# Kernel tuning notes

Hardware: AMD Instinct MI355X
Metric: run time of the kernel (lower is better)

The kernel has to match this reference:

```python
import jax, jax.numpy as jnp
import numpy as np


def _l2norm(t, eps=1e-12):
    # matches torch F.normalize(p=2, dim=-1): x / max(||x||_2, eps)
    n = jnp.sqrt(jnp.sum(t * t, axis=-1, keepdims=True))
    return t / jnp.maximum(n, eps)


def setup_inputs() -> dict:
    key = jax.random.key(0)
    ks = jax.random.split(key, 8)
    B, N, C, H, W = 16, 4, 256, 64, 64
    d = 64  # dim_head
    x = jax.random.normal(ks[0], (B, C, H, W), jnp.float32)
    fmaps = jax.random.normal(ks[1], (B, N, C, H, W), jnp.float32)
    Wq = jax.random.normal(ks[2], (N * d, C), jnp.float32) * 0.02   # Linear [out,in]
    Wk = jax.random.normal(ks[3], (N, d, C), jnp.float32) * 0.02    # grouped 1x1 conv, per-group [d,C]
    Wv = jax.random.normal(ks[4], (N, d, C), jnp.float32) * 0.02
    rescale = jnp.ones((N, 1, 1), jnp.float32)
    Wffn = jax.random.normal(ks[5], (C, N * d), jnp.float32) * 0.02
    bffn = jnp.zeros((C,), jnp.float32)
    return {"x": x, "fmaps": fmaps, "Wq": Wq, "Wk": Wk, "Wv": Wv,
            "rescale": rescale, "Wffn": Wffn, "bffn": bffn}


def reference(x, fmaps, Wq, Wk, Wv, rescale, Wffn, bffn):
    B, N, C, H, W = fmaps.shape
    d = Wk.shape[1]
    HW = H * W

    # x: [B,C,H,W] -> tokens [B,HW,C]
    x_in = jnp.transpose(x, (0, 2, 3, 1)).reshape(B, HW, C)
    q_in = jnp.einsum('bsc,oc->bso', x_in, Wq)            # [B,HW,N*d]

    # grouped 1x1 convs on fmaps (group = fmap index n)
    fm = fmaps.reshape(B, N, C, HW)                       # [B,N,C,HW]
    k = jnp.einsum('bncs,ndc->bnds', fm, Wk)              # [B,N,d,HW]
    v = jnp.einsum('bncs,ndc->bnds', fm, Wv)              # [B,N,d,HW]

    q = jnp.transpose(q_in.reshape(B, HW, N, d), (0, 2, 3, 1))  # [B,N,d,HW]

    qn = _l2norm(q)   # normalize over spatial (HW) axis
    kn = _l2norm(k)

    attn = jnp.einsum('bnds,bnes->bnde', kn, qn) * rescale      # [B,N,d,d]
    attn = jax.nn.softmax(attn, axis=-1)
    out = jnp.einsum('bnde,bnes->bnds', attn, v)                # [B,N,d,HW]

    out = jnp.transpose(out, (0, 3, 1, 2)).reshape(B, HW, N * d)  # [B,HW,N*d]
    out = out + q_in
    out = jnp.einsum('bsi,ci->bsc', out, Wffn) + bffn + q_in      # ffn + residual
    return jnp.transpose(out.reshape(B, H, W, C), (0, 3, 1, 2))   # [B,C,H,W]
```

## Files before the change

kernel.cpp:

```cpp
#include <hip/hip_runtime.h>
#include <hip/hip_bf16.h>
#include <cmath>

using bf16 = __hip_bfloat16;
typedef __attribute__((ext_vector_type(4))) float  f32x4;
typedef __attribute__((ext_vector_type(8))) short  bf16x8;
typedef unsigned int u32;
typedef unsigned short u16;

__device__ __forceinline__ void gl_lds16(const bf16* g, bf16* l) {
    __builtin_amdgcn_global_load_lds(
        (const __attribute__((address_space(1))) u32*)g,
        (__attribute__((address_space(3))) u32*)l, 16, 0, 0);
}

__device__ __forceinline__ u32 pk2(float a, float b) {
    bf16 ha = __float2bfloat16(a), hb = __float2bfloat16(b);
    return (u32)*(u16*)&ha | ((u32)*(u16*)&hb << 16);
}
__device__ __forceinline__ float b2f(u16 v) {
    return __uint_as_float((u32)v << 16);
}

__global__ __launch_bounds__(256) void qproj(
    const float* __restrict__ x,
    const bf16* __restrict__ Wq,
    bf16* __restrict__ qch)
{
    __shared__ bf16 sW[128 * 64];
    __shared__ bf16 sX[128 * 72];
    const int t = threadIdx.x;
    const int lane = t & 63, wid = t >> 6;
    const int wm = wid >> 1, wn = wid & 1;
    const int g = lane >> 4, lr = lane & 15;
    const int s0 = blockIdx.x * 128;
    const int o0 = blockIdx.y * 128;
    const float* xb = x + (long)blockIdx.z * 1048576;

    f32x4 acc[4][4];
#pragma unroll
    for (int i = 0; i < 4; ++i)
#pragma unroll
        for (int j = 0; j < 4; ++j) acc[i][j] = (f32x4){0.f, 0.f, 0.f, 0.f};

    const int p  = t & 31;
    const int sl = t >> 5;

    for (int c0 = 0; c0 < 256; c0 += 64) {
        __syncthreads();
#pragma unroll
        for (int i = 0; i < 4; ++i) {
            int lin = i * 256 + t, r = lin >> 3, ch = lin & 7;
            gl_lds16(Wq + (long)(o0 + r) * 256 + c0 + ((ch ^ (r & 7)) << 3), &sW[lin * 8]);
        }
#pragma unroll
        for (int j = 0; j < 4; ++j) {
            int s4 = j * 8 + sl;
            const float* src = xb + (long)(c0 + 2 * p) * 4096 + s0 + s4 * 4;
            float4 a = *(const float4*)src;
            float4 bq = *(const float4*)(src + 4096);
            char* base = (char*)sX + p * 4 + (s4 * 4) * 144;
            *(u32*)(base +   0) = pk2(a.x, bq.x);
            *(u32*)(base + 144) = pk2(a.y, bq.y);
            *(u32*)(base + 288) = pk2(a.z, bq.z);
            *(u32*)(base + 432) = pk2(a.w, bq.w);
        }
        __syncthreads();
#pragma unroll
        for (int kk = 0; kk < 2; ++kk) {
            bf16x8 aw[4], fx[4];
#pragma unroll
            for (int mf = 0; mf < 4; ++mf) {
                int r = wm * 64 + mf * 16 + lr;
                int ch = (kk * 4 + g) ^ (r & 7);
                aw[mf] = *(const bf16x8*)((const char*)sW + r * 128 + ch * 16);
            }
#pragma unroll
            for (int nf = 0; nf < 4; ++nf) {
                int s = wn * 64 + nf * 16 + lr;
                fx[nf] = *(const bf16x8*)((const char*)sX + s * 144 + (kk * 4 + g) * 16);
            }
#pragma unroll
            for (int mf = 0; mf < 4; ++mf)
#pragma unroll
                for (int nf = 0; nf < 4; ++nf)
                    acc[mf][nf] = __builtin_amdgcn_mfma_f32_16x16x32_bf16(
                        aw[mf], fx[nf], acc[mf][nf], 0, 0, 0);
        }
    }
    bf16* qb = qch + (long)blockIdx.z * 1048576;
#pragma unroll
    for (int mf = 0; mf < 4; ++mf)
#pragma unroll
        for (int nf = 0; nf < 4; ++nf)
#pragma unroll
            for (int e = 0; e < 4; ++e) {
                int o = o0 + wm * 64 + mf * 16 + g * 4 + e;
                int s = s0 + wn * 64 + nf * 16 + lr;
                qb[(long)o * 4096 + s] = __float2bfloat16(acc[mf][nf][e]);
            }
}

__global__ __launch_bounds__(256) void kvproj(
    const float* __restrict__ fm,
    const bf16* __restrict__ Wk,
    const bf16* __restrict__ Wv,
    bf16* __restrict__ kb,
    bf16* __restrict__ vT)
{
    __shared__ bf16 sF[128 * 72];
    __shared__ bf16 sK[64 * 64];
    __shared__ bf16 sV[64 * 64];
    const int t = threadIdx.x;
    const int lane = t & 63, wid = t >> 6;
    const int g = lane >> 4, lr = lane & 15;
    const int s0 = blockIdx.x * 128;
    const int bn = blockIdx.y, n = bn & 3;
    const float* fb = fm + (long)bn * 1048576;
    const bf16* WkN = Wk + (long)n * 16384;
    const bf16* WvN = Wv + (long)n * 16384;

    f32x4 acc1[4][2];
    f32x4 acc2[2][4];
#pragma unroll
    for (int i = 0; i < 4; ++i)
#pragma unroll
        for (int j = 0; j < 2; ++j) {
            acc1[i][j] = (f32x4){0.f, 0.f, 0.f, 0.f};
            acc2[j][i] = (f32x4){0.f, 0.f, 0.f, 0.f};
        }

    const int p  = t & 31;
    const int sl = t >> 5;

    for (int c0 = 0; c0 < 256; c0 += 64) {
        __syncthreads();
#pragma unroll
        for (int i = 0; i < 2; ++i) {
            int lin = i * 256 + t, r = lin >> 3, ch = lin & 7;
            int srcoff = r * 256 + c0 + ((ch ^ (r & 7)) << 3);
            gl_lds16(WkN + srcoff, &sK[lin * 8]);
            gl_lds16(WvN + srcoff, &sV[lin * 8]);
        }
#pragma unroll
        for (int j = 0; j < 4; ++j) {
            int s4 = j * 8 + sl;
            const float* src = fb + (long)(c0 + 2 * p) * 4096 + s0 + s4 * 4;
            float4 a = *(const float4*)src;
            float4 bq = *(const float4*)(src + 4096);
            char* base = (char*)sF + p * 4 + (s4 * 4) * 144;
            *(u32*)(base +   0) = pk2(a.x, bq.x);
            *(u32*)(base + 144) = pk2(a.y, bq.y);
            *(u32*)(base + 288) = pk2(a.z, bq.z);
            *(u32*)(base + 432) = pk2(a.w, bq.w);
        }
        __syncthreads();
#pragma unroll
        for (int kk = 0; kk < 2; ++kk) {
            bf16x8 ak[4], ff[2], bv[4];
#pragma unroll
            for (int mf = 0; mf < 4; ++mf) {
                int r = mf * 16 + lr;
                int ch = (kk * 4 + g) ^ (r & 7);
                ak[mf] = *(const bf16x8*)((const char*)sK + r * 128 + ch * 16);
            }
#pragma unroll
            for (int i = 0; i < 2; ++i) {
                int s = wid * 32 + i * 16 + lr;
                ff[i] = *(const bf16x8*)((const char*)sF + s * 144 + (kk * 4 + g) * 16);
            }
#pragma unroll
            for (int nf = 0; nf < 4; ++nf) {
                int r = nf * 16 + lr;
                int ch = (kk * 4 + g) ^ (r & 7);
                bv[nf] = *(const bf16x8*)((const char*)sV + r * 128 + ch * 16);
            }
#pragma unroll
            for (int mf = 0; mf < 4; ++mf)
#pragma unroll
                for (int i = 0; i < 2; ++i)
                    acc1[mf][i] = __builtin_amdgcn_mfma_f32_16x16x32_bf16(
                        ak[mf], ff[i], acc1[mf][i], 0, 0, 0);
#pragma unroll
            for (int i = 0; i < 2; ++i)
#pragma unroll
                for (int nf = 0; nf < 4; ++nf)
                    acc2[i][nf] = __builtin_amdgcn_mfma_f32_16x16x32_bf16(
                        ff[i], bv[nf], acc2[i][nf], 0, 0, 0);
        }
    }
    bf16* kbb = kb + (long)bn * 262144;
#pragma unroll
    for (int mf = 0; mf < 4; ++mf)
#pragma unroll
        for (int i = 0; i < 2; ++i)
#pragma unroll
            for (int e = 0; e < 4; ++e) {
                int dd = mf * 16 + g * 4 + e;
                int s  = s0 + wid * 32 + i * 16 + lr;
                kbb[(long)dd * 4096 + s] = __float2bfloat16(acc1[mf][i][e]);
            }
    bf16* vtb = vT + (long)bn * 262144;
#pragma unroll
    for (int i = 0; i < 2; ++i)
#pragma unroll
        for (int nf = 0; nf < 4; ++nf)
#pragma unroll
            for (int e = 0; e < 4; ++e) {
                int s = s0 + wid * 32 + i * 16 + g * 4 + e;
                int ec = nf * 16 + lr;
                vtb[(long)s * 64 + ec] = __float2bfloat16(acc2[i][nf][e]);
            }
}

__global__ __launch_bounds__(256) void qk_sum(
    const bf16* __restrict__ kb,
    const bf16* __restrict__ qch,
    float* __restrict__ part,
    float* __restrict__ sumq, float* __restrict__ sumk)
{
    __shared__ bf16 sA[64 * 64];
    __shared__ bf16 sB[64 * 64];
    const int t = threadIdx.x;
    const int lane = t & 63, wid = t >> 6;
    const int wm = wid >> 1, wn = wid & 1;
    const int g = lane >> 4, lr = lane & 15;
    const int ch_ = blockIdx.x;
    const int bn = blockIdx.y;
    const bf16* kbase = kb + (long)bn * 262144;
    const bf16* qbase = qch + (long)bn * 262144;

    const int srow = t >> 1;
    const int shalf = t & 1;

    f32x4 acc[2][2];
#pragma unroll
    for (int i = 0; i < 2; ++i)
#pragma unroll
        for (int j = 0; j < 2; ++j) acc[i][j] = (f32x4){0.f, 0.f, 0.f, 0.f};
    float ss = 0.f;

    for (int it = 0; it < 16; ++it) {
        int k0 = ch_ * 1024 + it * 64;
        __syncthreads();
#pragma unroll
        for (int i = 0; i < 2; ++i) {
            int lin = i * 256 + t, r = lin >> 3, c = lin & 7;
            gl_lds16(kbase + (long)r * 4096 + k0 + ((c ^ (r & 7)) << 3), &sA[lin * 8]);
            gl_lds16(qbase + (long)r * 4096 + k0 + ((c ^ (r & 7)) << 3), &sB[lin * 8]);
        }
        __syncthreads();
#pragma unroll
        for (int kk = 0; kk < 2; ++kk) {
            bf16x8 af[2], bf[2];
#pragma unroll
            for (int mf = 0; mf < 2; ++mf) {
                int r = wm * 32 + mf * 16 + lr;
                af[mf] = *(const bf16x8*)((const char*)sA + r * 128 + (((kk * 4 + g) ^ (r & 7)) << 4));
            }
#pragma unroll
            for (int nf = 0; nf < 2; ++nf) {
                int r = wn * 32 + nf * 16 + lr;
                bf[nf] = *(const bf16x8*)((const char*)sB + r * 128 + (((kk * 4 + g) ^ (r & 7)) << 4));
            }
#pragma unroll
            for (int mf = 0; mf < 2; ++mf)
#pragma unroll
                for (int nf = 0; nf < 2; ++nf)
                    acc[mf][nf] = __builtin_amdgcn_mfma_f32_16x16x32_bf16(
                        af[mf], bf[nf], acc[mf][nf], 0, 0, 0);
        }
        {
            const char* base = (srow < 64) ? (const char*)sA + srow * 128
                                           : (const char*)sB + (srow - 64) * 128;
            int r7 = srow & 7;
#pragma unroll
            for (int j = 0; j < 4; ++j) {
                bf16x8 v = *(const bf16x8*)(base + (((shalf * 4 + j) ^ r7) << 4));
#pragma unroll
                for (int e = 0; e < 8; ++e) {
                    float f = b2f((u16)v[e]);
                    ss += f * f;
                }
            }
        }
    }
    ss += __shfl_xor(ss, 1);
    if (shalf == 0) {
        if (srow < 64) atomicAdd(&sumk[bn * 64 + srow], ss);
        else           atomicAdd(&sumq[bn * 64 + srow - 64], ss);
    }
    float* pp = part + ((long)bn * 4 + ch_) * 4096;
#pragma unroll
    for (int mf = 0; mf < 2; ++mf)
#pragma unroll
        for (int nf = 0; nf < 2; ++nf)
#pragma unroll
            for (int e = 0; e < 4; ++e) {
                int m = wm * 32 + mf * 16 + g * 4 + e;
                int nn = wn * 32 + nf * 16 + lr;
                pp[m * 64 + nn] = acc[mf][nf][e];
            }
}

__global__ __launch_bounds__(256) void attn_finalize_kernel(
    const float* __restrict__ part,
    const float* __restrict__ sumq, const float* __restrict__ sumk,
    const float* __restrict__ rescale,
    bf16* __restrict__ attn_out)
{
    const int bn = blockIdx.x;
    const int n = bn & 3;
    const int t = threadIdx.x;
    const float rs = rescale[n];

    __shared__ float att[64][65];
    __shared__ float rmax[64], rsum[64];
    __shared__ float iq[64], ik[64];

    if (t < 64)        ik[t]      = 1.f / fmaxf(sqrtf(sumk[bn * 64 + t]), 1e-12f);
    else if (t < 128)  iq[t - 64] = 1.f / fmaxf(sqrtf(sumq[bn * 64 + t - 64]), 1e-12f);
    __syncthreads();

    const float* pb = part + (size_t)bn * 4 * 4096;
#pragma unroll
    for (int p = 0; p < 16; ++p) {
        int lin = p * 256 + t;
        int dd = lin >> 6, e = lin & 63;
        float v = pb[lin] + pb[4096 + lin] + pb[8192 + lin] + pb[12288 + lin];
        v *= ik[dd] * iq[e] * rs;
        att[dd][e] = v;
    }
    __syncthreads();
    if (t < 64) {
        float m = -1e30f;
        for (int e = 0; e < 64; ++e) m = fmaxf(m, att[t][e]);
        float sm = 0.f;
        for (int e = 0; e < 64; ++e) sm += expf(att[t][e] - m);
        rmax[t] = m;
        rsum[t] = 1.0f / sm;
    }
    __syncthreads();
    bf16* ob = attn_out + (size_t)bn * 4096;
#pragma unroll
    for (int p = 0; p < 16; ++p) {
        int lin = p * 256 + t;
        int dd = lin >> 6, e = lin & 63;
        ob[lin] = __float2bfloat16(expf(att[dd][e] - rmax[dd]) * rsum[dd]);
    }
}

__global__ __launch_bounds__(256) void pvffn(
    const bf16* __restrict__ vT,
    const bf16* __restrict__ attnb,
    const bf16* __restrict__ qch,
    const bf16* __restrict__ Wf,
    const float* __restrict__ bffn,
    float* __restrict__ out)
{
    __shared__ bf16 bufX[256 * 64];
    __shared__ bf16 Zs[128 * 64];
    const int t = threadIdx.x;
    const int lane = t & 63, wid = t >> 6;
    const int g = lane >> 4, lr = lane & 15;
    const int s0 = blockIdx.x * 128;
    const int b = blockIdx.y;

    f32x4 accF[4][8];
#pragma unroll
    for (int i = 0; i < 4; ++i)
#pragma unroll
        for (int j = 0; j < 8; ++j) accF[i][j] = (f32x4){0.f, 0.f, 0.f, 0.f};

    for (int n = 0; n < 4; ++n) {
        const int bn = b * 4 + n;
        __syncthreads();
#pragma unroll
        for (int i = 0; i < 4; ++i) {
            int lin = i * 256 + t, r = lin >> 3, c = lin & 7;
            gl_lds16(vT + (long)bn * 262144 + (long)(s0 + r) * 64 + ((c ^ (r & 7)) << 3),
                     &bufX[lin * 8]);
        }
#pragma unroll
        for (int i = 0; i < 2; ++i) {
            int lin = i * 256 + t, r = lin >> 3, c = lin & 7;
            gl_lds16(attnb + (long)bn * 4096 + r * 64 + ((c ^ (r & 7)) << 3),
                     &bufX[8192 + lin * 8]);
        }
        __syncthreads();
        f32x4 accP[2][4];
#pragma unroll
        for (int i = 0; i < 2; ++i)
#pragma unroll
            for (int j = 0; j < 4; ++j) accP[i][j] = (f32x4){0.f, 0.f, 0.f, 0.f};
#pragma unroll
        for (int kk = 0; kk < 2; ++kk) {
            bf16x8 av[2], at[4];
#pragma unroll
            for (int mf = 0; mf < 2; ++mf) {
                int r = wid * 32 + mf * 16 + lr;
                av[mf] = *(const bf16x8*)((const char*)bufX + r * 128 + (((kk * 4 + g) ^ (r & 7)) << 4));
            }
#pragma unroll
            for (int nf = 0; nf < 4; ++nf) {
                int r = nf * 16 + lr;
                at[nf] = *(const bf16x8*)((const char*)bufX + 16384 + r * 128 + (((kk * 4 + g) ^ (r & 7)) << 4));
            }
#pragma unroll
            for (int mf = 0; mf < 2; ++mf)
#pragma unroll
                for (int nf = 0; nf < 4; ++nf)
                    accP[mf][nf] = __builtin_amdgcn_mfma_f32_16x16x32_bf16(
                        av[mf], at[nf], accP[mf][nf], 0, 0, 0);
        }
#pragma unroll
        for (int mf = 0; mf < 2; ++mf)
#pragma unroll
            for (int nf = 0; nf < 4; ++nf) {
                int slb = wid * 32 + mf * 16 + g * 4;
                int il = nf * 16 + lr;
                ushort4 qv = *(const ushort4*)(qch + ((long)b * 256 + n * 64 + il) * 4096 + s0 + slb);
                u16 qa[4] = {qv.x, qv.y, qv.z, qv.w};
#pragma unroll
                for (int e = 0; e < 4; ++e) {
                    int sl = slb + e;
                    float v = accP[mf][nf][e] + b2f(qa[e]);
                    bf16 hv = __float2bfloat16(v);
                    int byte = sl * 128 + ((((il >> 3) ^ (sl & 7))) << 4) + (il & 7) * 2;
                    *(u16*)((char*)Zs + byte) = *(u16*)&hv;
                }
            }
        __syncthreads();
#pragma unroll
        for (int i = 0; i < 8; ++i) {
            int lin = i * 256 + t, r = lin >> 3, c = lin & 7;
            gl_lds16(Wf + (long)r * 256 + n * 64 + ((c ^ (r & 7)) << 3), &bufX[lin * 8]);
        }
        __syncthreads();
#pragma unroll
        for (int kk = 0; kk < 2; ++kk) {
            bf16x8 aw[4], bz[8];
#pragma unroll
            for (int mf = 0; mf < 4; ++mf) {
                int r = wid * 64 + mf * 16 + lr;
                aw[mf] = *(const bf16x8*)((const char*)bufX + r * 128 + (((kk * 4 + g) ^ (r & 7)) << 4));
            }
#pragma unroll
            for (int nf = 0; nf < 8; ++nf) {
                int sl = nf * 16 + lr;
                bz[nf] = *(const bf16x8*)((const char*)Zs + sl * 128 + (((kk * 4 + g) ^ (sl & 7)) << 4));
            }
#pragma unroll
            for (int mf = 0; mf < 4; ++mf)
#pragma unroll
                for (int nf = 0; nf < 8; ++nf)
                    accF[mf][nf] = __builtin_amdgcn_mfma_f32_16x16x32_bf16(
                        aw[mf], bz[nf], accF[mf][nf], 0, 0, 0);
        }
    }
    float* ob = out + (long)b * 1048576;
    const bf16* qb = qch + (long)b * 1048576;
#pragma unroll
    for (int mf = 0; mf < 4; ++mf)
#pragma unroll
        for (int e = 0; e < 4; ++e) {
            int c = wid * 64 + mf * 16 + g * 4 + e;
            float bv = bffn[c];
#pragma unroll
            for (int nf = 0; nf < 8; ++nf) {
                int s = s0 + nf * 16 + lr;
                long idx = (long)c * 4096 + s;
                ob[idx] = accF[mf][nf][e] + bv + b2f(*(const u16*)(qb + idx));
            }
        }
}

__global__ __launch_bounds__(256) void wconv(
    const float* __restrict__ a, const float* __restrict__ b,
    const float* __restrict__ c, const float* __restrict__ d,
    bf16* __restrict__ o)
{
    int i = blockIdx.x * 256 + threadIdx.x;
    int which = i >> 16, off = i & 65535;
    const float* s = (which == 0) ? a : (which == 1) ? b : (which == 2) ? c : d;
    o[i] = __float2bfloat16(s[off]);
}

extern "C" void kernel_launch(void* const* d_in, const int* in_sizes, int n_in,
                              void* d_out, int out_size, void* d_ws, size_t ws_size,
                              hipStream_t stream) {
    const float* x       = (const float*)d_in[0];
    const float* fmaps   = (const float*)d_in[1];
    const float* Wq      = (const float*)d_in[2];
    const float* Wk      = (const float*)d_in[3];
    const float* Wv      = (const float*)d_in[4];
    const float* rescale = (const float*)d_in[5];
    const float* Wffn    = (const float*)d_in[6];
    const float* bffn    = (const float*)d_in[7];
    float* out = (float*)d_out;

    char* w = (char*)d_ws;
    bf16* kbuf  = (bf16*)(w + 0);
    bf16* vT    = (bf16*)(w + 33554432L);
    bf16* qch   = (bf16*)(w + 67108864L);
    float* part = (float*)(w + 100663296L);
    bf16* attnb = (bf16*)(w + 104857600L);
    float* sumq = (float*)(w + 105381888L);
    float* sumk = (float*)(w + 105398272L);
    bf16* Wq_b  = (bf16*)(w + 105414656L);
    bf16* Wk_b  = Wq_b + 65536;
    bf16* Wv_b  = Wq_b + 131072;
    bf16* Wf_b  = Wq_b + 196608;

    dim3 blk(256);

    hipMemsetAsync(sumq, 0, 32768, stream);
    wconv<<<dim3(1024), blk, 0, stream>>>(Wq, Wk, Wv, Wffn, Wq_b);
    kvproj<<<dim3(32, 64), blk, 0, stream>>>(fmaps, Wk_b, Wv_b, kbuf, vT);
    qproj<<<dim3(32, 2, 16), blk, 0, stream>>>(x, Wq_b, qch);
    qk_sum<<<dim3(4, 64), blk, 0, stream>>>(kbuf, qch, part, sumq, sumk);
    attn_finalize_kernel<<<dim3(64), blk, 0, stream>>>(part, sumq, sumk, rescale, attnb);
    pvffn<<<dim3(32, 16), blk, 0, stream>>>(vT, attnb, qch, Wf_b, bffn, out);
}
```

Before: 200.9 us.

## Double-buffer LDS tiles across projection, QK and PV/FFN kernels

Adds ping-pong shared-memory buffers to qproj, kvproj, qk_sum and pvffn so the next channel or spatial chunk is fetched while MFMAs run on the current one. qk_sum now splits its reduction 8 ways and writes per-chunk partial norms instead of using atomics, which removes the memset; finalize sums the chunks. pvffn loads Wffn fragments straight into registers rather than staging them through LDS. The cost is more LDS per block, which may lower occupancy, plus more register pressure.

```diff
diff --git a/kernel.cpp b/kernel.cpp
--- a/kernel.cpp
+++ b/kernel.cpp
@@ -27,8 +27,8 @@
     const bf16* __restrict__ Wq,
     bf16* __restrict__ qch)
 {
-    __shared__ bf16 sW[128 * 64];
-    __shared__ bf16 sX[128 * 72];
+    __shared__ bf16 sW[2][128 * 64];
+    __shared__ bf16 sX[2][128 * 72];
     const int t = threadIdx.x;
     const int lane = t & 63, wid = t >> 6;
     const int wm = wid >> 1, wn = wid & 1;
@@ -46,39 +46,62 @@
     const int p  = t & 31;
     const int sl = t >> 5;
 
-    for (int c0 = 0; c0 < 256; c0 += 64) {
-        __syncthreads();
+    {
 #pragma unroll
         for (int i = 0; i < 4; ++i) {
             int lin = i * 256 + t, r = lin >> 3, ch = lin & 7;
-            gl_lds16(Wq + (long)(o0 + r) * 256 + c0 + ((ch ^ (r & 7)) << 3), &sW[lin * 8]);
-        }
+            gl_lds16(Wq + (long)(o0 + r) * 256 + ((ch ^ (r & 7)) << 3), &sW[0][lin * 8]);
+        }
+        float4 ra[4], rb[4];
 #pragma unroll
         for (int j = 0; j < 4; ++j) {
-            int s4 = j * 8 + sl;
-            const float* src = xb + (long)(c0 + 2 * p) * 4096 + s0 + s4 * 4;
-            float4 a = *(const float4*)src;
-            float4 bq = *(const float4*)(src + 4096);
-            char* base = (char*)sX + p * 4 + (s4 * 4) * 144;
-            *(u32*)(base +   0) = pk2(a.x, bq.x);
-            *(u32*)(base + 144) = pk2(a.y, bq.y);
-            *(u32*)(base + 288) = pk2(a.z, bq.z);
-            *(u32*)(base + 432) = pk2(a.w, bq.w);
+            const float* src = xb + (long)(2 * p) * 4096 + s0 + (j * 8 + sl) * 4;
+            ra[j] = *(const float4*)src;
+            rb[j] = *(const float4*)(src + 4096);
+        }
+#pragma unroll
+        for (int j = 0; j < 4; ++j) {
+            char* base = (char*)&sX[0][0] + p * 4 + ((j * 8 + sl) * 4) * 144;
+            *(u32*)(base +   0) = pk2(ra[j].x, rb[j].x);
+            *(u32*)(base + 144) = pk2(ra[j].y, rb[j].y);
+            *(u32*)(base + 288) = pk2(ra[j].z, rb[j].z);
+            *(u32*)(base + 432) = pk2(ra[j].w, rb[j].w);
         }
         __syncthreads();
+    }
+
+    int cur = 0;
+    for (int it = 0; it < 4; ++it) {
+        const int c0n = (it + 1) * 64;
+        float4 ra[4], rb[4];
+        if (it < 3) {
+#pragma unroll
+            for (int i = 0; i < 4; ++i) {
+                int lin = i * 256 + t, r = lin >> 3, ch = lin & 7;
+                gl_lds16(Wq + (long)(o0 + r) * 256 + c0n + ((ch ^ (r & 7)) << 3),
+                         &sW[cur ^ 1][lin * 8]);
+            }
+#pragma unroll
+            for (int j = 0; j < 4; ++j) {
+                const float* src = xb + (long)(c0n + 2 * p) * 4096 + s0 + (j * 8 + sl) * 4;
+                ra[j] = *(const float4*)src;
+                rb[j] = *(const float4*)(src + 4096);
+            }
+        }
+        const char* wbase = (const char*)&sW[cur][0];
+        const char* xbase = (const char*)&sX[cur][0];
 #pragma unroll
         for (int kk = 0; kk < 2; ++kk) {
             bf16x8 aw[4], fx[4];
 #pragma unroll
             for (int mf = 0; mf < 4; ++mf) {
                 int r = wm * 64 + mf * 16 + lr;
-                int ch = (kk * 4 + g) ^ (r & 7);
-                aw[mf] = *(const bf16x8*)((const char*)sW + r * 128 + ch * 16);
+                aw[mf] = *(const bf16x8*)(wbase + r * 128 + (((kk * 4 + g) ^ (r & 7)) << 4));
             }
 #pragma unroll
             for (int nf = 0; nf < 4; ++nf) {
                 int s = wn * 64 + nf * 16 + lr;
-                fx[nf] = *(const bf16x8*)((const char*)sX + s * 144 + (kk * 4 + g) * 16);
+                fx[nf] = *(const bf16x8*)(xbase + s * 144 + (kk * 4 + g) * 16);
             }
 #pragma unroll
             for (int mf = 0; mf < 4; ++mf)
@@ -87,7 +110,20 @@
                     acc[mf][nf] = __builtin_amdgcn_mfma_f32_16x16x32_bf16(
                         aw[mf], fx[nf], acc[mf][nf], 0, 0, 0);
         }
-    }
+        if (it < 3) {
+#pragma unroll
+            for (int j = 0; j < 4; ++j) {
+                char* base = (char*)&sX[cur ^ 1][0] + p * 4 + ((j * 8 + sl) * 4) * 144;
+                *(u32*)(base +   0) = pk2(ra[j].x, rb[j].x);
+                *(u32*)(base + 144) = pk2(ra[j].y, rb[j].y);
+                *(u32*)(base + 288) = pk2(ra[j].z, rb[j].z);
+                *(u32*)(base + 432) = pk2(ra[j].w, rb[j].w);
+            }
+            __syncthreads();
+            cur ^= 1;
+        }
+    }
+
     bf16* qb = qch + (long)blockIdx.z * 1048576;
 #pragma unroll
     for (int mf = 0; mf < 4; ++mf)
@@ -108,9 +144,9 @@
     bf16* __restrict__ kb,
     bf16* __restrict__ vT)
 {
-    __shared__ bf16 sF[128 * 72];
-    __shared__ bf16 sK[64 * 64];
-    __shared__ bf16 sV[64 * 64];
+    __shared__ bf16 sF[2][128 * 72];
+    __shared__ bf16 sK[2][64 * 64];
+    __shared__ bf16 sV[2][64 * 64];
     const int t = threadIdx.x;
     const int lane = t & 63, wid = t >> 6;
     const int g = lane >> 4, lr = lane & 15;
@@ -133,47 +169,71 @@
     const int p  = t & 31;
     const int sl = t >> 5;
 
-    for (int c0 = 0; c0 < 256; c0 += 64) {
-        __syncthreads();
+    {
 #pragma unroll
         for (int i = 0; i < 2; ++i) {
             int lin = i * 256 + t, r = lin >> 3, ch = lin & 7;
-            int srcoff = r * 256 + c0 + ((ch ^ (r & 7)) << 3);
-            gl_lds16(WkN + srcoff, &sK[lin * 8]);
-            gl_lds16(WvN + srcoff, &sV[lin * 8]);
-        }
+            int off = r * 256 + ((ch ^ (r & 7)) << 3);
+            gl_lds16(WkN + off, &sK[0][lin * 8]);
+            gl_lds16(WvN + off, &sV[0][lin * 8]);
+        }
+        float4 ra[4], rb[4];
 #pragma unroll
         for (int j = 0; j < 4; ++j) {
-            int s4 = j * 8 + sl;
-            const float* src = fb + (long)(c0 + 2 * p) * 4096 + s0 + s4 * 4;
-            float4 a = *(const float4*)src;
-            float4 bq = *(const float4*)(src + 4096);
-            char* base = (char*)sF + p * 4 + (s4 * 4) * 144;
-            *(u32*)(base +   0) = pk2(a.x, bq.x);
-            *(u32*)(base + 144) = pk2(a.y, bq.y);
-            *(u32*)(base + 288) = pk2(a.z, bq.z);
-            *(u32*)(base + 432) = pk2(a.w, bq.w);
+            const float* src = fb + (long)(2 * p) * 4096 + s0 + (j * 8 + sl) * 4;
+            ra[j] = *(const float4*)src;
+            rb[j] = *(const float4*)(src + 4096);
+        }
+#pragma unroll
+        for (int j = 0; j < 4; ++j) {
+            char* base = (char*)&sF[0][0] + p * 4 + ((j * 8 + sl) * 4) * 144;
+            *(u32*)(base +   0) = pk2(ra[j].x, rb[j].x);
+            *(u32*)(base + 144) = pk2(ra[j].y, rb[j].y);
+            *(u32*)(base + 288) = pk2(ra[j].z, rb[j].z);
+            *(u32*)(base + 432) = pk2(ra[j].w, rb[j].w);
         }
         __syncthreads();
+    }
+
+    int cur = 0;
+    for (int it = 0; it < 4; ++it) {
+        const int c0n = (it + 1) * 64;
+        float4 ra[4], rb[4];
+        if (it < 3) {
+#pragma unroll
+            for (int i = 0; i < 2; ++i) {
+                int lin = i * 256 + t, r = lin >> 3, ch = lin & 7;
+                int off = r * 256 + c0n + ((ch ^ (r & 7)) << 3);
+                gl_lds16(WkN + off, &sK[cur ^ 1][lin * 8]);
+                gl_lds16(WvN + off, &sV[cur ^ 1][lin * 8]);
+            }
+#pragma unroll
+            for (int j = 0; j < 4; ++j) {
+                const float* src = fb + (long)(c0n + 2 * p) * 4096 + s0 + (j * 8 + sl) * 4;
+                ra[j] = *(const float4*)src;
+                rb[j] = *(const float4*)(src + 4096);
+            }
+        }
+        const char* fbase = (const char*)&sF[cur][0];
+        const char* kbase = (const char*)&sK[cur][0];
+        const char* vbase = (const char*)&sV[cur][0];
 #pragma unroll
         for (int kk = 0; kk < 2; ++kk) {
             bf16x8 ak[4], ff[2], bv[4];
 #pragma unroll
             for (int mf = 0; mf < 4; ++mf) {
                 int r = mf * 16 + lr;
-                int ch = (kk * 4 + g) ^ (r & 7);
-                ak[mf] = *(const bf16x8*)((const char*)sK + r * 128 + ch * 16);
+                ak[mf] = *(const bf16x8*)(kbase + r * 128 + (((kk * 4 + g) ^ (r & 7)) << 4));
             }
 #pragma unroll
             for (int i = 0; i < 2; ++i) {
                 int s = wid * 32 + i * 16 + lr;
-                ff[i] = *(const bf16x8*)((const char*)sF + s * 144 + (kk * 4 + g) * 16);
+                ff[i] = *(const bf16x8*)(fbase + s * 144 + (kk * 4 + g) * 16);
             }
 #pragma unroll
             for (int nf = 0; nf < 4; ++nf) {
                 int r = nf * 16 + lr;
-                int ch = (kk * 4 + g) ^ (r & 7);
-                bv[nf] = *(const bf16x8*)((const char*)sV + r * 128 + ch * 16);
+                bv[nf] = *(const bf16x8*)(vbase + r * 128 + (((kk * 4 + g) ^ (r & 7)) << 4));
             }
 #pragma unroll
             for (int mf = 0; mf < 4; ++mf)
@@ -188,7 +248,20 @@
                     acc2[i][nf] = __builtin_amdgcn_mfma_f32_16x16x32_bf16(
                         ff[i], bv[nf], acc2[i][nf], 0, 0, 0);
         }
-    }
+        if (it < 3) {
+#pragma unroll
+            for (int j = 0; j < 4; ++j) {
+                char* base = (char*)&sF[cur ^ 1][0] + p * 4 + ((j * 8 + sl) * 4) * 144;
+                *(u32*)(base +   0) = pk2(ra[j].x, rb[j].x);
+                *(u32*)(base + 144) = pk2(ra[j].y, rb[j].y);
+                *(u32*)(base + 288) = pk2(ra[j].z, rb[j].z);
+                *(u32*)(base + 432) = pk2(ra[j].w, rb[j].w);
+            }
+            __syncthreads();
+            cur ^= 1;
+        }
+    }
+
     bf16* kbb = kb + (long)bn * 262144;
 #pragma unroll
     for (int mf = 0; mf < 4; ++mf)
@@ -219,8 +292,8 @@
     float* __restrict__ part,
     float* __restrict__ sumq, float* __restrict__ sumk)
 {
-    __shared__ bf16 sA[64 * 64];
-    __shared__ bf16 sB[64 * 64];
+    __shared__ bf16 sA[2][64 * 64];
+    __shared__ bf16 sB[2][64 * 64];
     const int t = threadIdx.x;
     const int lane = t & 63, wid = t >> 6;
     const int wm = wid >> 1, wn = wid & 1;
@@ -240,28 +313,42 @@
         for (int j = 0; j < 2; ++j) acc[i][j] = (f32x4){0.f, 0.f, 0.f, 0.f};
     float ss = 0.f;
 
-    for (int it = 0; it < 16; ++it) {
-        int k0 = ch_ * 1024 + it * 64;
-        __syncthreads();
+    {
+        int k0 = ch_ * 512;
 #pragma unroll
         for (int i = 0; i < 2; ++i) {
             int lin = i * 256 + t, r = lin >> 3, c = lin & 7;
-            gl_lds16(kbase + (long)r * 4096 + k0 + ((c ^ (r & 7)) << 3), &sA[lin * 8]);
-            gl_lds16(qbase + (long)r * 4096 + k0 + ((c ^ (r & 7)) << 3), &sB[lin * 8]);
+            gl_lds16(kbase + (long)r * 4096 + k0 + ((c ^ (r & 7)) << 3), &sA[0][lin * 8]);
+            gl_lds16(qbase + (long)r * 4096 + k0 + ((c ^ (r & 7)) << 3), &sB[0][lin * 8]);
         }
         __syncthreads();
+    }
+
+    int cur = 0;
+    for (int it = 0; it < 8; ++it) {
+        if (it < 7) {
+            int k0 = ch_ * 512 + (it + 1) * 64;
+#pragma unroll
+            for (int i = 0; i < 2; ++i) {
+                int lin = i * 256 + t, r = lin >> 3, c = lin & 7;
+                gl_lds16(kbase + (long)r * 4096 + k0 + ((c ^ (r & 7)) << 3), &sA[cur ^ 1][lin * 8]);
+                gl_lds16(qbase + (long)r * 4096 + k0 + ((c ^ (r & 7)) << 3), &sB[cur ^ 1][lin * 8]);
+            }
+        }
+        const char* abase = (const char*)&sA[cur][0];
+        const char* bbase = (const char*)&sB[cur][0];
 #pragma unroll
         for (int kk = 0; kk < 2; ++kk) {
             bf16x8 af[2], bf[2];
 #pragma unroll
             for (int mf = 0; mf < 2; ++mf) {
                 int r = wm * 32 + mf * 16 + lr;
-                af[mf] = *(const bf16x8*)((const char*)sA + r * 128 + (((kk * 4 + g) ^ (r & 7)) << 4));
+                af[mf] = *(const bf16x8*)(abase + r * 128 + (((kk * 4 + g) ^ (r & 7)) << 4));
             }
 #pragma unroll
             for (int nf = 0; nf < 2; ++nf) {
                 int r = wn * 32 + nf * 16 + lr;
-                bf[nf] = *(const bf16x8*)((const char*)sB + r * 128 + (((kk * 4 + g) ^ (r & 7)) << 4));
+                bf[nf] = *(const bf16x8*)(bbase + r * 128 + (((kk * 4 + g) ^ (r & 7)) << 4));
             }
 #pragma unroll
             for (int mf = 0; mf < 2; ++mf)
@@ -271,8 +358,8 @@
                         af[mf], bf[nf], acc[mf][nf], 0, 0, 0);
         }
         {
-            const char* base = (srow < 64) ? (const char*)sA + srow * 128
-                                           : (const char*)sB + (srow - 64) * 128;
+            const char* base = (srow < 64) ? abase + srow * 128
+                                           : bbase + (srow - 64) * 128;
             int r7 = srow & 7;
 #pragma unroll
             for (int j = 0; j < 4; ++j) {
@@ -284,13 +371,16 @@
                 }
             }
         }
-    }
+        __syncthreads();
+        cur ^= 1;
+    }
+
     ss += __shfl_xor(ss, 1);
     if (shalf == 0) {
-        if (srow < 64) atomicAdd(&sumk[bn * 64 + srow], ss);
-        else           atomicAdd(&sumq[bn * 64 + srow - 64], ss);
-    }
-    float* pp = part + ((long)bn * 4 + ch_) * 4096;
+        if (srow < 64) sumk[ch_ * 4096 + bn * 64 + srow] = ss;
+        else           sumq[ch_ * 4096 + bn * 64 + srow - 64] = ss;
+    }
+    float* pp = part + ((long)bn * 8 + ch_) * 4096;
 #pragma unroll
     for (int mf = 0; mf < 2; ++mf)
 #pragma unroll
@@ -318,16 +408,27 @@
     __shared__ float rmax[64], rsum[64];
     __shared__ float iq[64], ik[64];
 
-    if (t < 64)        ik[t]      = 1.f / fmaxf(sqrtf(sumk[bn * 64 + t]), 1e-12f);
-    else if (t < 128)  iq[t - 64] = 1.f / fmaxf(sqrtf(sumq[bn * 64 + t - 64]), 1e-12f);
+    if (t < 64) {
+        float s = 0.f;
+#pragma unroll
+        for (int c = 0; c < 8; ++c) s += sumk[c * 4096 + bn * 64 + t];
+        ik[t] = 1.f / fmaxf(sqrtf(s), 1e-12f);
+    } else if (t < 128) {
+        float s = 0.f;
+#pragma unroll
+        for (int c = 0; c < 8; ++c) s += sumq[c * 4096 + bn * 64 + t - 64];
+        iq[t - 64] = 1.f / fmaxf(sqrtf(s), 1e-12f);
+    }
     __syncthreads();
 
-    const float* pb = part + (size_t)bn * 4 * 4096;
+    const float* pb = part + (size_t)bn * 8 * 4096;
 #pragma unroll
     for (int p = 0; p < 16; ++p) {
         int lin = p * 256 + t;
         int dd = lin >> 6, e = lin & 63;
-        float v = pb[lin] + pb[4096 + lin] + pb[8192 + lin] + pb[12288 + lin];
+        float v = 0.f;
+#pragma unroll
+        for (int c = 0; c < 8; ++c) v += pb[c * 4096 + lin];
         v *= ik[dd] * iq[e] * rs;
         att[dd][e] = v;
     }
@@ -358,7 +459,7 @@
     const float* __restrict__ bffn,
     float* __restrict__ out)
 {
-    __shared__ bf16 bufX[256 * 64];
+    __shared__ bf16 bufA[2][12288];
     __shared__ bf16 Zs[128 * 64];
     const int t = threadIdx.x;
     const int lane = t & 63, wid = t >> 6;
@@ -372,22 +473,51 @@
 #pragma unroll
         for (int j = 0; j < 8; ++j) accF[i][j] = (f32x4){0.f, 0.f, 0.f, 0.f};
 
-    for (int n = 0; n < 4; ++n) {
-        const int bn = b * 4 + n;
-        __syncthreads();
+    {
+        const int bn = b * 4;
 #pragma unroll
         for (int i = 0; i < 4; ++i) {
             int lin = i * 256 + t, r = lin >> 3, c = lin & 7;
             gl_lds16(vT + (long)bn * 262144 + (long)(s0 + r) * 64 + ((c ^ (r & 7)) << 3),
-                     &bufX[lin * 8]);
+                     &bufA[0][lin * 8]);
         }
 #pragma unroll
         for (int i = 0; i < 2; ++i) {
             int lin = i * 256 + t, r = lin >> 3, c = lin & 7;
             gl_lds16(attnb + (long)bn * 4096 + r * 64 + ((c ^ (r & 7)) << 3),
-                     &bufX[8192 + lin * 8]);
+                     &bufA[0][8192 + lin * 8]);
         }
         __syncthreads();
+    }
+
+    for (int n = 0; n < 4; ++n) {
+        const int bn = b * 4 + n;
+        const int cur = n & 1;
+        if (n < 3) {
+            const int bnn = bn + 1;
+#pragma unroll
+            for (int i = 0; i < 4; ++i) {
+                int lin = i * 256 + t, r = lin >> 3, c = lin & 7;
+                gl_lds16(vT + (long)bnn * 262144 + (long)(s0 + r) * 64 + ((c ^ (r & 7)) << 3),
+                         &bufA[cur ^ 1][lin * 8]);
+            }
+#pragma unroll
+            for (int i = 0; i < 2; ++i) {
+                int lin = i * 256 + t, r = lin >> 3, c = lin & 7;
+                gl_lds16(attnb + (long)bnn * 4096 + r * 64 + ((c ^ (r & 7)) << 3),
+                         &bufA[cur ^ 1][8192 + lin * 8]);
+            }
+        }
+        bf16x8 wf[2][4];
+#pragma unroll
+        for (int kk = 0; kk < 2; ++kk)
+#pragma unroll
+            for (int mf = 0; mf < 4; ++mf)
+                wf[kk][mf] = *(const bf16x8*)(
+                    Wf + (long)(wid * 64 + mf * 16 + lr) * 256 + n * 64 + (kk * 4 + g) * 8);
+
+        const char* vb = (const char*)&bufA[cur][0];
+        const char* ab = vb + 16384;
         f32x4 accP[2][4];
 #pragma unroll
         for (int i = 0; i < 2; ++i)
@@ -399,12 +529,12 @@
 #pragma unroll
             for (int mf = 0; mf < 2; ++mf) {
                 int r = wid * 32 + mf * 16 + lr;
-                av[mf] = *(const bf16x8*)((const char*)bufX + r * 128 + (((kk * 4 + g) ^ (r & 7)) << 4));
+                av[mf] = *(const bf16x8*)(vb + r * 128 + (((kk * 4 + g) ^ (r & 7)) << 4));
             }
 #pragma unroll
             for (int nf = 0; nf < 4; ++nf) {
                 int r = nf * 16 + lr;
-                at[nf] = *(const bf16x8*)((const char*)bufX + 16384 + r * 128 + (((kk * 4 + g) ^ (r & 7)) << 4));
+                at[nf] = *(const bf16x8*)(ab + r * 128 + (((kk * 4 + g) ^ (r & 7)) << 4));
             }
 #pragma unroll
             for (int mf = 0; mf < 2; ++mf)
@@ -432,19 +562,8 @@
             }
         __syncthreads();
 #pragma unroll
-        for (int i = 0; i < 8; ++i) {
-            int lin = i * 256 + t, r = lin >> 3, c = lin & 7;
-            gl_lds16(Wf + (long)r * 256 + n * 64 + ((c ^ (r & 7)) << 3), &bufX[lin * 8]);
-        }
-        __syncthreads();
-#pragma unroll
         for (int kk = 0; kk < 2; ++kk) {
-            bf16x8 aw[4], bz[8];
-#pragma unroll
-            for (int mf = 0; mf < 4; ++mf) {
-                int r = wid * 64 + mf * 16 + lr;
-                aw[mf] = *(const bf16x8*)((const char*)bufX + r * 128 + (((kk * 4 + g) ^ (r & 7)) << 4));
-            }
+            bf16x8 bz[8];
 #pragma unroll
             for (int nf = 0; nf < 8; ++nf) {
                 int sl = nf * 16 + lr;
@@ -455,9 +574,11 @@
 #pragma unroll
                 for (int nf = 0; nf < 8; ++nf)
                     accF[mf][nf] = __builtin_amdgcn_mfma_f32_16x16x32_bf16(
-                        aw[mf], bz[nf], accF[mf][nf], 0, 0, 0);
-        }
-    }
+                        wf[kk][mf], bz[nf], accF[mf][nf], 0, 0, 0);
+        }
+        __syncthreads();
+    }
+
     float* ob = out + (long)b * 1048576;
     const bf16* qb = qch + (long)b * 1048576;
 #pragma unroll
@@ -504,21 +625,20 @@
     bf16* vT    = (bf16*)(w + 33554432L);
     bf16* qch   = (bf16*)(w + 67108864L);
     float* part = (float*)(w + 100663296L);
-    bf16* attnb = (bf16*)(w + 104857600L);
-    float* sumq = (float*)(w + 105381888L);
-    float* sumk = (float*)(w + 105398272L);
-    bf16* Wq_b  = (bf16*)(w + 105414656L);
+    bf16* attnb = (bf16*)(w + 109051904L);
+    float* sumq = (float*)(w + 109576192L);
+    float* sumk = (float*)(w + 109707264L);
+    bf16* Wq_b  = (bf16*)(w + 109838336L);
     bf16* Wk_b  = Wq_b + 65536;
     bf16* Wv_b  = Wq_b + 131072;
     bf16* Wf_b  = Wq_b + 196608;
 
     dim3 blk(256);
 
-    hipMemsetAsync(sumq, 0, 32768, stream);
     wconv<<<dim3(1024), blk, 0, stream>>>(Wq, Wk, Wv, Wffn, Wq_b);
     kvproj<<<dim3(32, 64), blk, 0, stream>>>(fmaps, Wk_b, Wv_b, kbuf, vT);
     qproj<<<dim3(32, 2, 16), blk, 0, stream>>>(x, Wq_b, qch);
-    qk_sum<<<dim3(4, 64), blk, 0, stream>>>(kbuf, qch, part, sumq, sumk);
+    qk_sum<<<dim3(8, 64), blk, 0, stream>>>(kbuf, qch, part, sumq, sumk);
     attn_finalize_kernel<<<dim3(64), blk, 0, stream>>>(part, sumq, sumk, rescale, attnb);
     pvffn<<<dim3(32, 16), blk, 0, stream>>>(vT, attnb, qch, Wf_b, bffn, out);
 }
```

Result: faster. 194.2 us (-3.4%).
